# Optimization experiments

Hardware: AMD Instinct MI355X
Metric: run time of the kernel (lower is better)

The kernel has to match this reference:

```python
import jax, jax.numpy as jnp
import numpy as np

PAD_IDX = 0
NEG_INF = -1e30

N_USERS, N_ITEMS, N_SUBJECTS, EMB_DIM = 100000, 100000, 10000, 16
B, L = 16384, 50


def setup_inputs() -> dict:
    key = jax.random.key(0)
    ks = jax.random.split(key, 10)
    subj_emb = jax.random.normal(ks[0], (N_SUBJECTS, EMB_DIM), dtype=jnp.float32) * 0.1
    subj_emb = subj_emb.at[PAD_IDX].set(0.0)  # padding_idx row is zeros in torch
    attn_w = jax.random.normal(ks[1], (EMB_DIM,), dtype=jnp.float32) * 0.25
    attn_b = jnp.zeros((), dtype=jnp.float32)
    user_bias = jax.random.normal(ks[2], (N_USERS,), dtype=jnp.float32) * 0.05
    item_bias = jax.random.normal(ks[3], (N_ITEMS,), dtype=jnp.float32) * 0.05
    global_bias = jnp.zeros((), dtype=jnp.float32)
    user_idx = jax.random.randint(ks[4], (B,), 0, N_USERS)
    item_idx = jax.random.randint(ks[5], (B,), 0, N_ITEMS)
    fav_subjects = jax.random.randint(ks[6], (B, L), 0, N_SUBJECTS)
    book_subjects = jax.random.randint(ks[7], (B, L), 0, N_SUBJECTS)
    return {
        "subj_emb": subj_emb, "attn_w": attn_w, "attn_b": attn_b,
        "user_bias": user_bias, "item_bias": item_bias, "global_bias": global_bias,
        "user_idx": user_idx, "item_idx": item_idx,
        "fav_subjects": fav_subjects, "book_subjects": book_subjects,
    }


def attention_pool(indices, subj_emb, attn_w, attn_b):
    embs = subj_emb[indices]                      # [B, L, D] gather
    scores = embs @ attn_w + attn_b               # [B, L] tiny linear (D->1)
    mask = indices != PAD_IDX                     # [B, L]
    has_real = jnp.any(mask, axis=1)              # [B]
    # rows with no real subjects get position 0 unmasked (torch per-row loop)
    safe_mask = mask.at[:, 0].set(mask[:, 0] | ~has_real)
    scores = jnp.where(safe_mask, scores, NEG_INF)
    weights = jax.nn.softmax(scores, axis=1)      # [B, L]
    pooled = jnp.einsum("bld,bl->bd", embs, weights)
    return pooled  # dropout is identity in eval mode


def reference(subj_emb, attn_w, attn_b, user_bias, item_bias, global_bias,
              user_idx, item_idx, fav_subjects, book_subjects):
    u_emb = attention_pool(fav_subjects, subj_emb, attn_w, attn_b)   # [B, D]
    i_emb = attention_pool(book_subjects, subj_emb, attn_w, attn_b)  # [B, D]
    dot = jnp.sum(u_emb * i_emb, axis=1)                             # [B]
    return dot + user_bias[user_idx] + item_bias[item_idx] + global_bias
```

## Files before the change

kernel.cpp:

```cpp
#include <hip/hip_runtime.h>
#include <math.h>


#define PAD_IDX 0
constexpr int D = 16;
constexpr int ROWS_PER_BLOCK = 8;
constexpr int THREADS = 256;

__global__ __launch_bounds__(256) void exp_table_kernel(
    const float* __restrict__ subj_emb,
    const float* __restrict__ attn_w,
    const float* __restrict__ attn_b,
    float* __restrict__ exptab,
    int n_subj)
{
    const int s = blockIdx.x * blockDim.x + threadIdx.x;
    if (s >= n_subj) return;
    const float4* e = (const float4*)(subj_emb + (long)s * D);
    const float4* w = (const float4*)attn_w;
    float4 e0 = e[0], e1 = e[1], e2 = e[2], e3 = e[3];
    float4 w0 = w[0], w1 = w[1], w2 = w[2], w3 = w[3];
    float acc = e0.x * w0.x + e0.y * w0.y + e0.z * w0.z + e0.w * w0.w
              + e1.x * w1.x + e1.y * w1.y + e1.z * w1.z + e1.w * w1.w
              + e2.x * w2.x + e2.y * w2.y + e2.z * w2.z + e2.w * w2.w
              + e3.x * w3.x + e3.y * w3.y + e3.z * w3.z + e3.w * w3.w;
    exptab[s] = __expf(acc + attn_b[0]);
}

template <int LFIX>
__global__ __launch_bounds__(256) void pool_kernel(
    const float* __restrict__ subj_emb,
    const float* __restrict__ exptab,
    const float* __restrict__ user_bias,
    const float* __restrict__ item_bias,
    const float* __restrict__ global_bias,
    const int*  __restrict__ user_idx,
    const int*  __restrict__ item_idx,
    const int*  __restrict__ fav_subjects,
    const int*  __restrict__ book_subjects,
    float* __restrict__ out,
    int B)
{
    __shared__ int sidx[2][ROWS_PER_BLOCK * LFIX];

    const int row0  = blockIdx.x * ROWS_PER_BLOCK;
    const int nInts = ROWS_PER_BLOCK * LFIX;
    const long base = (long)row0 * LFIX;

    {
        const int n4 = nInts >> 2;
        const int4* fsrc = (const int4*)(fav_subjects  + base);
        const int4* bsrc = (const int4*)(book_subjects + base);
        int4* fdst = (int4*)sidx[0];
        int4* bdst = (int4*)sidx[1];
        for (int i = threadIdx.x; i < n4; i += THREADS) {
            fdst[i] = fsrc[i];
            bdst[i] = bsrc[i];
        }
        for (int i = (n4 << 2) + threadIdx.x; i < nInts; i += THREADS) {
            sidx[0][i] = fav_subjects[base + i];
            sidx[1][i] = book_subjects[base + i];
        }
    }
    __syncthreads();

    const int t    = threadIdx.x;
    const int r    = t >> 5;
    const int c    = (t >> 3) & 3;
    const int pool = (t >> 2) & 1;
    const int j    = t & 3;
    const int row  = row0 + r;

    const int* __restrict__ idxl = sidx[pool] + r * LFIX;

    float4 acc = {0.f, 0.f, 0.f, 0.f};
    float  s   = 0.f;

    constexpr int ITERS = (LFIX + 3) / 4;
    #pragma unroll
    for (int k = 0; k < ITERS; ++k) {
        const int l  = c + 4 * k;
        const int si = (l < LFIX) ? idxl[l] : PAD_IDX;
        const float ew = exptab[si];
        const float4 e = *(const float4*)(subj_emb + (long)si * D + 4 * j);
        const float w = (si != PAD_IDX) ? ew : 0.f;
        s     += w;
        acc.x += w * e.x;
        acc.y += w * e.y;
        acc.z += w * e.z;
        acc.w += w * e.w;
    }

    acc.x += __shfl_xor(acc.x, 8, 32);  acc.x += __shfl_xor(acc.x, 16, 32);
    acc.y += __shfl_xor(acc.y, 8, 32);  acc.y += __shfl_xor(acc.y, 16, 32);
    acc.z += __shfl_xor(acc.z, 8, 32);  acc.z += __shfl_xor(acc.z, 16, 32);
    acc.w += __shfl_xor(acc.w, 8, 32);  acc.w += __shfl_xor(acc.w, 16, 32);
    s     += __shfl_xor(s,     8, 32);  s     += __shfl_xor(s,     16, 32);

    const float inv = (s > 0.f) ? (1.f / s) : 0.f;
    float4 u;
    u.x = acc.x * inv; u.y = acc.y * inv; u.z = acc.z * inv; u.w = acc.w * inv;

    float4 o;
    o.x = __shfl_xor(u.x, 4, 8);
    o.y = __shfl_xor(u.y, 4, 8);
    o.z = __shfl_xor(u.z, 4, 8);
    o.w = __shfl_xor(u.w, 4, 8);

    float prod = u.x * o.x + u.y * o.y + u.z * o.z + u.w * o.w;
    prod += __shfl_xor(prod, 1, 4);
    prod += __shfl_xor(prod, 2, 4);

    if (row < B && (t & 31) == 0) {
        out[row] = prod + user_bias[user_idx[row]]
                        + item_bias[item_idx[row]]
                        + global_bias[0];
    }
}

__global__ __launch_bounds__(256) void pool_kernel_gen(
    const float* __restrict__ subj_emb,
    const float* __restrict__ exptab,
    const float* __restrict__ user_bias,
    const float* __restrict__ item_bias,
    const float* __restrict__ global_bias,
    const int*  __restrict__ user_idx,
    const int*  __restrict__ item_idx,
    const int*  __restrict__ fav_subjects,
    const int*  __restrict__ book_subjects,
    float* __restrict__ out,
    int B, int L)
{
    __shared__ int sidx[2][ROWS_PER_BLOCK * 128];
    const int row0  = blockIdx.x * ROWS_PER_BLOCK;
    const int nInts = ROWS_PER_BLOCK * L;
    const long base = (long)row0 * L;
    for (int i = threadIdx.x; i < nInts; i += THREADS) {
        sidx[0][i] = fav_subjects[base + i];
        sidx[1][i] = book_subjects[base + i];
    }
    __syncthreads();

    const int t    = threadIdx.x;
    const int r    = t >> 5;
    const int c    = (t >> 3) & 3;
    const int pool = (t >> 2) & 1;
    const int j    = t & 3;
    const int row  = row0 + r;
    const int* __restrict__ idxl = sidx[pool] + r * L;

    float4 acc = {0.f, 0.f, 0.f, 0.f};
    float  s   = 0.f;
    for (int l = c; l < L; l += 4) {
        const int si = idxl[l];
        const float ew = exptab[si];
        const float4 e = *(const float4*)(subj_emb + (long)si * D + 4 * j);
        const float w = (si != PAD_IDX) ? ew : 0.f;
        s += w;
        acc.x += w * e.x; acc.y += w * e.y; acc.z += w * e.z; acc.w += w * e.w;
    }
    acc.x += __shfl_xor(acc.x, 8, 32);  acc.x += __shfl_xor(acc.x, 16, 32);
    acc.y += __shfl_xor(acc.y, 8, 32);  acc.y += __shfl_xor(acc.y, 16, 32);
    acc.z += __shfl_xor(acc.z, 8, 32);  acc.z += __shfl_xor(acc.z, 16, 32);
    acc.w += __shfl_xor(acc.w, 8, 32);  acc.w += __shfl_xor(acc.w, 16, 32);
    s     += __shfl_xor(s,     8, 32);  s     += __shfl_xor(s,     16, 32);
    const float inv = (s > 0.f) ? (1.f / s) : 0.f;
    float4 u = {acc.x * inv, acc.y * inv, acc.z * inv, acc.w * inv};
    float4 o;
    o.x = __shfl_xor(u.x, 4, 8); o.y = __shfl_xor(u.y, 4, 8);
    o.z = __shfl_xor(u.z, 4, 8); o.w = __shfl_xor(u.w, 4, 8);
    float prod = u.x * o.x + u.y * o.y + u.z * o.z + u.w * o.w;
    prod += __shfl_xor(prod, 1, 4);
    prod += __shfl_xor(prod, 2, 4);
    if (row < B && (t & 31) == 0) {
        out[row] = prod + user_bias[user_idx[row]]
                        + item_bias[item_idx[row]] + global_bias[0];
    }
}

extern "C" void kernel_launch(void* const* d_in, const int* in_sizes, int n_in,
                              void* d_out, int out_size, void* d_ws, size_t ws_size,
                              hipStream_t stream) {
    const float* subj_emb    = (const float*)d_in[0];
    const float* attn_w      = (const float*)d_in[1];
    const float* attn_b      = (const float*)d_in[2];
    const float* user_bias   = (const float*)d_in[3];
    const float* item_bias   = (const float*)d_in[4];
    const float* global_bias = (const float*)d_in[5];
    const int*   user_idx    = (const int*)d_in[6];
    const int*   item_idx    = (const int*)d_in[7];
    const int*   fav_subj    = (const int*)d_in[8];
    const int*   book_subj   = (const int*)d_in[9];
    float*       out         = (float*)d_out;
    float*       exptab      = (float*)d_ws;

    const int n_subj = in_sizes[0] / D;
    const int B      = in_sizes[6];
    const int L      = in_sizes[8] / B;

    {
        const int blocks = (n_subj + 255) / 256;
        exp_table_kernel<<<blocks, 256, 0, stream>>>(
            subj_emb, attn_w, attn_b, exptab, n_subj);
    }
    const int blocks = (B + ROWS_PER_BLOCK - 1) / ROWS_PER_BLOCK;
    if (L == 50) {
        pool_kernel<50><<<blocks, THREADS, 0, stream>>>(
            subj_emb, exptab, user_bias, item_bias, global_bias,
            user_idx, item_idx, fav_subj, book_subj, out, B);
    } else {
        pool_kernel_gen<<<blocks, THREADS, 0, stream>>>(
            subj_emb, exptab, user_bias, item_bias, global_bias,
            user_idx, item_idx, fav_subj, book_subj, out, B, L);
    }
}
```

Before: 89.63 us.

## Fuse exp-score table into pool kernel, computing scores inline via shuffles

Removes the separate kernel that precomputed exp(emb·w+b) per subject and the per-element gather from that table. Each pooling thread now computes a partial dot product of its embedding slice with the attention weights, reduces across the 4-lane group with shuffles, and takes the exp inline. This saves one kernel launch and one dependent random gather per element. In exchange it adds shuffles and recomputes the exp for every lookup instead of once per subject.

After: 85.39 us. -4.7%, faster.

```diff
diff --git a/kernel.cpp b/kernel.cpp
--- a/kernel.cpp
+++ b/kernel.cpp
@@ -7,30 +7,11 @@
 constexpr int ROWS_PER_BLOCK = 8;
 constexpr int THREADS = 256;
 
-__global__ __launch_bounds__(256) void exp_table_kernel(
+template <int LFIX>
+__global__ __launch_bounds__(256) void pool_kernel(
     const float* __restrict__ subj_emb,
     const float* __restrict__ attn_w,
     const float* __restrict__ attn_b,
-    float* __restrict__ exptab,
-    int n_subj)
-{
-    const int s = blockIdx.x * blockDim.x + threadIdx.x;
-    if (s >= n_subj) return;
-    const float4* e = (const float4*)(subj_emb + (long)s * D);
-    const float4* w = (const float4*)attn_w;
-    float4 e0 = e[0], e1 = e[1], e2 = e[2], e3 = e[3];
-    float4 w0 = w[0], w1 = w[1], w2 = w[2], w3 = w[3];
-    float acc = e0.x * w0.x + e0.y * w0.y + e0.z * w0.z + e0.w * w0.w
-              + e1.x * w1.x + e1.y * w1.y + e1.z * w1.z + e1.w * w1.w
-              + e2.x * w2.x + e2.y * w2.y + e2.z * w2.z + e2.w * w2.w
-              + e3.x * w3.x + e3.y * w3.y + e3.z * w3.z + e3.w * w3.w;
-    exptab[s] = __expf(acc + attn_b[0]);
-}
-
-template <int LFIX>
-__global__ __launch_bounds__(256) void pool_kernel(
-    const float* __restrict__ subj_emb,
-    const float* __restrict__ exptab,
     const float* __restrict__ user_bias,
     const float* __restrict__ item_bias,
     const float* __restrict__ global_bias,
@@ -71,6 +52,9 @@
     const int j    = t & 3;
     const int row  = row0 + r;
 
+    const float4 wv = *(const float4*)(attn_w + 4 * j);
+    const float  bb = attn_b[0];
+
     const int* __restrict__ idxl = sidx[pool] + r * LFIX;
 
     float4 acc = {0.f, 0.f, 0.f, 0.f};
@@ -81,9 +65,12 @@
     for (int k = 0; k < ITERS; ++k) {
         const int l  = c + 4 * k;
         const int si = (l < LFIX) ? idxl[l] : PAD_IDX;
-        const float ew = exptab[si];
         const float4 e = *(const float4*)(subj_emb + (long)si * D + 4 * j);
-        const float w = (si != PAD_IDX) ? ew : 0.f;
+        float p = e.x * wv.x + e.y * wv.y + e.z * wv.z + e.w * wv.w;
+        p += __shfl_xor(p, 1, 4);
+        p += __shfl_xor(p, 2, 4);
+        const float ew = __expf(p + bb);
+        const float w  = (si != PAD_IDX) ? ew : 0.f;
         s     += w;
         acc.x += w * e.x;
         acc.y += w * e.y;
@@ -120,7 +107,8 @@
 
 __global__ __launch_bounds__(256) void pool_kernel_gen(
     const float* __restrict__ subj_emb,
-    const float* __restrict__ exptab,
+    const float* __restrict__ attn_w,
+    const float* __restrict__ attn_b,
     const float* __restrict__ user_bias,
     const float* __restrict__ item_bias,
     const float* __restrict__ global_bias,
@@ -147,15 +135,20 @@
     const int pool = (t >> 2) & 1;
     const int j    = t & 3;
     const int row  = row0 + r;
+    const float4 wv = *(const float4*)(attn_w + 4 * j);
+    const float  bb = attn_b[0];
     const int* __restrict__ idxl = sidx[pool] + r * L;
 
     float4 acc = {0.f, 0.f, 0.f, 0.f};
     float  s   = 0.f;
     for (int l = c; l < L; l += 4) {
         const int si = idxl[l];
-        const float ew = exptab[si];
         const float4 e = *(const float4*)(subj_emb + (long)si * D + 4 * j);
-        const float w = (si != PAD_IDX) ? ew : 0.f;
+        float p = e.x * wv.x + e.y * wv.y + e.z * wv.z + e.w * wv.w;
+        p += __shfl_xor(p, 1, 4);
+        p += __shfl_xor(p, 2, 4);
+        const float ew = __expf(p + bb);
+        const float w  = (si != PAD_IDX) ? ew : 0.f;
         s += w;
         acc.x += w * e.x; acc.y += w * e.y; acc.z += w * e.z; acc.w += w * e.w;
     }
@@ -192,25 +185,20 @@
     const int*   fav_subj    = (const int*)d_in[8];
     const int*   book_subj   = (const int*)d_in[9];
     float*       out         = (float*)d_out;
-    float*       exptab      = (float*)d_ws;
-
-    const int n_subj = in_sizes[0] / D;
-    const int B      = in_sizes[6];
-    const int L      = in_sizes[8] / B;
-
-    {
-        const int blocks = (n_subj + 255) / 256;
-        exp_table_kernel<<<blocks, 256, 0, stream>>>(
-            subj_emb, attn_w, attn_b, exptab, n_subj);
-    }
+
+    const int D_ = 16;
+    const int B  = in_sizes[6];
+    const int L  = in_sizes[8] / B;
+    (void)D_; (void)d_ws; (void)ws_size;
+
     const int blocks = (B + ROWS_PER_BLOCK - 1) / ROWS_PER_BLOCK;
     if (L == 50) {
         pool_kernel<50><<<blocks, THREADS, 0, stream>>>(
-            subj_emb, exptab, user_bias, item_bias, global_bias,
+            subj_emb, attn_w, attn_b, user_bias, item_bias, global_bias,
             user_idx, item_idx, fav_subj, book_subj, out, B);
     } else {
         pool_kernel_gen<<<blocks, THREADS, 0, stream>>>(
-            subj_emb, exptab, user_bias, item_bias, global_bias,
+            subj_emb, attn_w, attn_b, user_bias, item_bias, global_bias,
             user_idx, item_idx, fav_subj, book_subj, out, B, L);
     }
 }
```
